# Performance work log

Measured on AMD Instinct MI355X. Metric: run time of the kernel, lower is better.

The kernel has to match this reference:

```python
import jax, jax.numpy as jnp
import numpy as np

H = 12
DH = 64
R = 8
LN_EPS = 1e-12


def setup_inputs() -> dict:
    key = jax.random.key(0)
    ks = jax.random.split(key, 6)
    B, T, D = 32, 512, 768
    s = 0.02  # realistic init scale so softmax/LN stay well-conditioned
    return {
        "hidden_states": jax.random.normal(ks[0], (B, T, D), jnp.float32),
        "Wq": jax.random.normal(ks[1], (D, D), jnp.float32) * s,
        "bq": jnp.zeros((D,), jnp.float32),
        "Wk": jax.random.normal(ks[2], (D, D), jnp.float32) * s,
        "bk": jnp.zeros((D,), jnp.float32),
        "Wv": jax.random.normal(ks[3], (D, D), jnp.float32) * s,
        "bv": jnp.zeros((D,), jnp.float32),
        "Wo": jax.random.normal(ks[4], (D, D), jnp.float32) * s,
        "bo": jnp.zeros((D,), jnp.float32),
        "ln_g": jnp.ones((D,), jnp.float32),
        "ln_b": jnp.zeros((D,), jnp.float32),
    }


def _bipartite_indices(metric, r):
    # metric: (B, T, dh); cosine-sim bipartite matching between even (a) and odd (b) tokens
    m = metric / (jnp.linalg.norm(metric, axis=-1, keepdims=True) + 1e-6)
    a, b = m[:, ::2], m[:, 1::2]
    scores = jnp.einsum('bad,bcd->bac', a, b)  # (B, Ta, Tb)
    node_max = scores.max(axis=-1)
    node_idx = scores.argmax(axis=-1)
    node_max = node_max.at[:, 0].set(-jnp.inf)  # protect CLS (a[0])
    r = min(r, a.shape[1] - 1)
    sorted_idx = jnp.argsort(-node_max, axis=-1)  # descending
    src_idx = sorted_idx[:, :r]
    unm_idx = sorted_idx[:, r:]
    dst_idx = jnp.take_along_axis(node_idx, src_idx, axis=-1)
    return src_idx, unm_idx, dst_idx


def _merge(x, src_idx, unm_idx, dst_idx):
    # x: (B, T, C) -> (B, T - r, C); scatter-mean matched even tokens into odd tokens
    src, dst = x[:, ::2], x[:, 1::2]
    matched = jnp.take_along_axis(src, src_idx[:, :, None], axis=1)  # (B, r, C)

    def scat(d, di, mm):
        sums = jnp.zeros_like(d).at[di].add(mm)
        cnt = jnp.zeros((d.shape[0],), d.dtype).at[di].add(jnp.ones(di.shape, d.dtype))
        # torch scatter_reduce 'mean' with include_self=True: (self + sum) / (1 + count)
        return (d + sums) / (1.0 + cnt[:, None])

    dst = jax.vmap(scat)(dst, dst_idx, matched)
    unm = jnp.take_along_axis(src, unm_idx[:, :, None], axis=1)
    return jnp.concatenate([unm, dst], axis=1)


def reference(hidden_states, Wq, bq, Wk, bk, Wv, bv, Wo, bo, ln_g, ln_b):
    B, T, D = hidden_states.shape

    def split_heads(x):
        return x.reshape(B, T, H, DH).transpose(0, 2, 1, 3)  # (B, H, T, dh)

    residual = hidden_states
    q = split_heads(hidden_states @ Wq + bq)
    k = split_heads(hidden_states @ Wk + bk)
    v = split_heads(hidden_states @ Wv + bv)

    # ToMe: match on head-averaged keys (computed under no_grad in torch)
    metric = jax.lax.stop_gradient(k.mean(axis=1))  # (B, T, dh)
    src_idx, unm_idx, dst_idx = _bipartite_indices(metric, R)

    def merge_heads(x):
        Bx, Hx, Tx, dx = x.shape
        y = x.transpose(0, 2, 1, 3).reshape(Bx, Tx, Hx * dx)
        y = _merge(y, src_idx, unm_idx, dst_idx)
        return y.reshape(Bx, y.shape[1], Hx, dx).transpose(0, 2, 1, 3)

    q = merge_heads(q)
    k = merge_heads(k)
    v = merge_heads(v)
    residual = _merge(residual, src_idx, unm_idx, dst_idx)

    scores = jnp.einsum('bhqd,bhkd->bhqk', q, k) / jnp.sqrt(jnp.float32(DH))
    probs = jax.nn.softmax(scores, axis=-1)  # dropout is identity in eval
    ctx = jnp.einsum('bhqk,bhkd->bhqd', probs, v)
    T2 = ctx.shape[2]
    ctx = ctx.transpose(0, 2, 1, 3).reshape(B, T2, D)
    out = ctx @ Wo + bo

    x = out + residual
    mu = x.mean(axis=-1, keepdims=True)
    var = x.var(axis=-1, keepdims=True)
    return (x - mu) / jnp.sqrt(var + LN_EPS) * ln_g + ln_b
```

## Files before the change

### kernel.cpp

```cpp
#include <hip/hip_runtime.h>
#include <math.h>

#define BNUM 32
#define TT   512
#define DD   768
#define HH   12
#define DHH  64
#define RR   8
#define TSRC 256
#define UNM  248
#define TM   504
#define MROW 16128

typedef unsigned short u16;
typedef unsigned int   u32;
typedef __attribute__((ext_vector_type(8))) short bfrag;
typedef __attribute__((ext_vector_type(4))) float ffrag;

__device__ __forceinline__ u16 f2bf(float f) {
  u32 u = __float_as_uint(f);
  u = (u + 0x7fffu + ((u >> 16) & 1u)) >> 16;
  return (u16)u;
}
__device__ __forceinline__ u32 pack2bf(float a, float b) {
  u32 ua = __float_as_uint(a), ub = __float_as_uint(b);
  ua += 0x7fffu + ((ua >> 16) & 1u);
  ub += 0x7fffu + ((ub >> 16) & 1u);
  return (ua >> 16) | (ub & 0xffff0000u);
}
__device__ __forceinline__ float bf2f(u16 v) {
  return __uint_as_float(((u32)v) << 16);
}

__device__ __forceinline__ void gl2lds16(const u16* g, u16* l) {
  __builtin_amdgcn_global_load_lds(
      (const __attribute__((address_space(1))) void*)(g),
      (__attribute__((address_space(3))) void*)(l), 16, 0, 0);
}

__global__ __launch_bounds__(256) void wkr_kernel(
    const float* __restrict__ Wk, const float* __restrict__ bk,
    float* __restrict__ Wkr, float* __restrict__ bkr) {
  int idx = blockIdx.x * 256 + threadIdx.x;
  int d = idx >> 6, j = idx & 63;
  float s = 0.f;
  #pragma unroll
  for (int h = 0; h < HH; ++h) s += Wk[(size_t)d * DD + h * DHH + j];
  Wkr[idx] = s * (1.f / 12.f);
  if (idx < 64) {
    float sb = 0.f;
    #pragma unroll
    for (int h = 0; h < HH; ++h) sb += bk[h * DHH + idx];
    bkr[idx] = sb * (1.f / 12.f);
  }
}

__global__ __launch_bounds__(256) void gemm_f32_kernel(
    const float* __restrict__ A, const float* __restrict__ W,
    const float* __restrict__ bias, float* __restrict__ C,
    int M, int N, int K) {
  __shared__ float As[32][68];
  __shared__ float Ws[32][68];
  const int t  = threadIdx.x;
  const int m0 = blockIdx.x * 64;
  const int tx = t & 15, ty = t >> 4;
  const int a_kk = t & 31;
  const int a_m  = t >> 5;
  const int w_n  = t & 63;
  const int w_k0 = t >> 6;

  float a_pre[8], w_pre[8];
  #pragma unroll
  for (int l = 0; l < 8; ++l)
    a_pre[l] = A[(size_t)(m0 + a_m + 8 * l) * K + a_kk];
  #pragma unroll
  for (int l = 0; l < 8; ++l)
    w_pre[l] = W[(size_t)(w_k0 * 8 + l) * N + w_n];

  float acc[4][4];
  #pragma unroll
  for (int i = 0; i < 4; ++i)
    #pragma unroll
    for (int j = 0; j < 4; ++j) acc[i][j] = 0.f;

  for (int k0 = 0; k0 < K; k0 += 32) {
    __syncthreads();
    #pragma unroll
    for (int l = 0; l < 8; ++l) As[a_kk][a_m + 8 * l] = a_pre[l];
    #pragma unroll
    for (int l = 0; l < 8; ++l) Ws[w_k0 * 8 + l][w_n] = w_pre[l];
    __syncthreads();
    if (k0 + 32 < K) {
      #pragma unroll
      for (int l = 0; l < 8; ++l)
        a_pre[l] = A[(size_t)(m0 + a_m + 8 * l) * K + k0 + 32 + a_kk];
      #pragma unroll
      for (int l = 0; l < 8; ++l)
        w_pre[l] = W[(size_t)(k0 + 32 + w_k0 * 8 + l) * N + w_n];
    }
    #pragma unroll
    for (int kk = 0; kk < 32; ++kk) {
      float4 a4 = *(const float4*)&As[kk][ty * 4];
      float4 w4 = *(const float4*)&Ws[kk][tx * 4];
      acc[0][0] += a4.x * w4.x; acc[0][1] += a4.x * w4.y;
      acc[0][2] += a4.x * w4.z; acc[0][3] += a4.x * w4.w;
      acc[1][0] += a4.y * w4.x; acc[1][1] += a4.y * w4.y;
      acc[1][2] += a4.y * w4.z; acc[1][3] += a4.y * w4.w;
      acc[2][0] += a4.z * w4.x; acc[2][1] += a4.z * w4.y;
      acc[2][2] += a4.z * w4.z; acc[2][3] += a4.z * w4.w;
      acc[3][0] += a4.w * w4.x; acc[3][1] += a4.w * w4.y;
      acc[3][2] += a4.w * w4.z; acc[3][3] += a4.w * w4.w;
    }
  }
  const float4 b4 = *(const float4*)&bias[tx * 4];
  #pragma unroll
  for (int i = 0; i < 4; ++i) {
    float4 v;
    v.x = acc[i][0] + b4.x; v.y = acc[i][1] + b4.y;
    v.z = acc[i][2] + b4.z; v.w = acc[i][3] + b4.w;
    *(float4*)&C[(size_t)(m0 + ty * 4 + i) * N + tx * 4] = v;
  }
}

__global__ __launch_bounds__(256) void wconv_kernel(
    const float* __restrict__ W0, const float* __restrict__ W1,
    const float* __restrict__ W2, const float* __restrict__ W3,
    u16* __restrict__ T0, u16* __restrict__ T1,
    u16* __restrict__ T2, u16* __restrict__ T3) {
  __shared__ float tile[64][65];
  int wi = blockIdx.z;
  const float* W = (wi == 0) ? W0 : (wi == 1) ? W1 : (wi == 2) ? W2 : W3;
  u16* T = (wi == 0) ? T0 : (wi == 1) ? T1 : (wi == 2) ? T2 : T3;
  int k0 = blockIdx.x * 64, n0 = blockIdx.y * 64;
  int t = threadIdx.x;
  int r = t >> 2, c4 = (t & 3) * 16;
  #pragma unroll
  for (int j = 0; j < 16; j += 4) {
    float4 v = *(const float4*)&W[(size_t)(k0 + r) * DD + n0 + c4 + j];
    tile[r][c4 + j] = v.x; tile[r][c4 + j + 1] = v.y;
    tile[r][c4 + j + 2] = v.z; tile[r][c4 + j + 3] = v.w;
  }
  __syncthreads();
  #pragma unroll
  for (int j = 0; j < 16; j += 2) {
    u32 p = (u32)f2bf(tile[c4 + j][r]) | ((u32)f2bf(tile[c4 + j + 1][r]) << 16);
    *(u32*)&T[(size_t)(n0 + r) * DD + k0 + c4 + j] = p;
  }
}

template <bool OUT_BF16, bool ADD_RES, bool ROW_BIAS, bool QK>
__global__ __launch_bounds__(256, 4) void mfma_gemm_kernel(
    const u16* __restrict__ A, const u16* __restrict__ BT,
    const float* __restrict__ bias, const float* __restrict__ bias2,
    const float* __restrict__ Res,
    float* __restrict__ Cf, u16* __restrict__ Cb, u16* __restrict__ Cb2,
    int M, int N, int K) {
  __shared__ u16 Als[2][128 * 32];
  __shared__ u16 Bls[2][128 * 32];
  const int t  = threadIdx.x;

  const int nwg = gridDim.x * gridDim.y;
  int id = blockIdx.x + blockIdx.y * gridDim.x;
  {
    const int qq = nwg >> 3, rr = nwg & 7;
    const int xcd = id & 7, pos = id >> 3;
    id = (xcd < rr) ? (xcd * (qq + 1) + pos)
                    : (rr * (qq + 1) + (xcd - rr) * qq + pos);
  }
  const int m0 = (id % gridDim.x) * 128;
  const int n0 = (id / gridDim.x) * 128;

  const int lane = t & 63;
  const int w  = t >> 6;
  const int wm = w & 1, wn = w >> 1;
  const int q  = lane >> 4;
  const int lr = lane & 15;

  const int srow = lane >> 2;
  const int schk = (lane & 3) ^ ((lane >> 3) & 3);
  const u16* gA = A  + (size_t)(m0 + w * 32 + srow) * K + schk * 8;
  const u16* gB = BT + (size_t)(n0 + w * 32 + srow) * K + schk * 8;

  const int ceff = q ^ ((lr >> 1) & 3);

  const float* biasp = bias;
  u16* Cbp = Cb;
  int n0c = n0;
  if (QK && n0 >= DD) { biasp = bias2; Cbp = Cb2; n0c = n0 - DD; }

  ffrag acc[4][4];
  #pragma unroll
  for (int i = 0; i < 4; ++i)
    #pragma unroll
    for (int j = 0; j < 4; ++j) {
      acc[i][j].x = 0.f; acc[i][j].y = 0.f; acc[i][j].z = 0.f; acc[i][j].w = 0.f;
    }

  auto STAGE = [&](int buf, int k0) {
    #pragma unroll
    for (int i = 0; i < 2; ++i) {
      gl2lds16(gA + (size_t)(i * 16) * K + k0, &Als[buf][(w * 32 + i * 16) * 32]);
      gl2lds16(gB + (size_t)(i * 16) * K + k0, &Bls[buf][(w * 32 + i * 16) * 32]);
    }
  };

  STAGE(0, 0);
  __syncthreads();

  const int NK = K >> 5;
  for (int kt = 0; kt < NK; ++kt) {
    const int cur = kt & 1;
    if (kt + 1 < NK) STAGE(cur ^ 1, (kt + 1) << 5);

    bfrag af[4], bfv[4];
    #pragma unroll
    for (int mi = 0; mi < 4; ++mi)
      af[mi] = *(const bfrag*)&Als[cur][((wm * 4 + mi) * 64 + lr * 4 + ceff) * 8];
    #pragma unroll
    for (int ni = 0; ni < 4; ++ni)
      bfv[ni] = *(const bfrag*)&Bls[cur][((wn * 4 + ni) * 64 + lr * 4 + ceff) * 8];
    #pragma unroll
    for (int mi = 0; mi < 4; ++mi)
      #pragma unroll
      for (int ni = 0; ni < 4; ++ni)
        acc[mi][ni] = __builtin_amdgcn_mfma_f32_16x16x32_bf16(
            af[mi], bfv[ni], acc[mi][ni], 0, 0, 0);

    __syncthreads();
  }

  float bcol[4];
  if (!ROW_BIAS) {
    #pragma unroll
    for (int ni = 0; ni < 4; ++ni)
      bcol[ni] = biasp[n0c + wn * 64 + ni * 16 + lr];
  }

  #pragma unroll
  for (int mi = 0; mi < 4; ++mi) {
    #pragma unroll
    for (int ni = 0; ni < 4; ++ni) {
      int gcol = n0c + wn * 64 + ni * 16 + lr;
      #pragma unroll
      for (int r = 0; r < 4; ++r) {
        int grow = m0 + wm * 64 + mi * 16 + q * 4 + r;
        size_t off = (size_t)grow * N + gcol;
        float v = acc[mi][ni][r];
        v += ROW_BIAS ? bias[grow] : bcol[ni];
        if (ADD_RES) v += Res[off];
        if (OUT_BF16) Cbp[off] = f2bf(v);
        else          Cf[off] = v;
      }
    }
  }
}

__global__ __launch_bounds__(256) void tome_scores_kernel(
    const float* __restrict__ metric, float* __restrict__ node_max,
    int* __restrict__ node_idx) {
  __shared__ float Bs[128][68];
  const int blk = blockIdx.x;
  const int b = blk >> 3, g = blk & 7;
  const int t = threadIdx.x;
  const int r = t >> 3, cc = t & 7;
  const int arow = g * 32 + r;
  const float* Mb = metric + (size_t)b * TT * 64;

  float areg[64];
  float na = 0.f;
  #pragma unroll
  for (int d4 = 0; d4 < 16; ++d4) {
    float4 v = *(const float4*)&Mb[(size_t)(2 * arow) * 64 + d4 * 4];
    areg[4 * d4 + 0] = v.x; areg[4 * d4 + 1] = v.y;
    areg[4 * d4 + 2] = v.z; areg[4 * d4 + 3] = v.w;
    na += v.x * v.x; na += v.y * v.y; na += v.z * v.z; na += v.w * v.w;
  }
  float ia = 1.f / (sqrtf(na) + 1e-6f);
  #pragma unroll
  for (int d = 0; d < 64; ++d) areg[d] *= ia;

  float best = -INFINITY; int besti = 0;
  for (int p = 0; p < 2; ++p) {
    __syncthreads();
    if (t < 128) {
      int c = p * 128 + t;
      const float* src = &Mb[(size_t)(2 * c + 1) * 64];
      float nb = 0.f;
      #pragma unroll
      for (int d4 = 0; d4 < 16; ++d4) {
        float4 v = *(const float4*)&src[d4 * 4];
        *(float4*)&Bs[t][d4 * 4] = v;
        nb += v.x * v.x; nb += v.y * v.y; nb += v.z * v.z; nb += v.w * v.w;
      }
      float ib = 1.f / (sqrtf(nb) + 1e-6f);
      #pragma unroll
      for (int d4 = 0; d4 < 16; ++d4) {
        float4 v = *(float4*)&Bs[t][d4 * 4];
        v.x *= ib; v.y *= ib; v.z *= ib; v.w *= ib;
        *(float4*)&Bs[t][d4 * 4] = v;
      }
    }
    __syncthreads();
    for (int j = 0; j < 16; ++j) {
      int cl = cc + 8 * j;
      float s = 0.f;
      #pragma unroll
      for (int d4 = 0; d4 < 16; ++d4) {
        float4 bv = *(const float4*)&Bs[cl][d4 * 4];
        s += areg[4 * d4 + 0] * bv.x; s += areg[4 * d4 + 1] * bv.y;
        s += areg[4 * d4 + 2] * bv.z; s += areg[4 * d4 + 3] * bv.w;
      }
      int c = p * 128 + cl;
      if (s > best) { best = s; besti = c; }
    }
  }
  #pragma unroll
  for (int off = 1; off < 8; off <<= 1) {
    float bm = __shfl_xor(best, off);
    int   bi = __shfl_xor(besti, off);
    if (bm > best || (bm == best && bi < besti)) { best = bm; besti = bi; }
  }
  if (cc == 0) {
    node_max[b * TSRC + arow] = best;
    node_idx[b * TSRC + arow] = besti;
  }
}

__global__ __launch_bounds__(256) void tome_rank_kernel(
    const float* __restrict__ node_max, const int* __restrict__ node_idx,
    int* __restrict__ order_g, int* __restrict__ dst_g) {
  __shared__ float km[TSRC];
  __shared__ int ord[TSRC];
  int b = blockIdx.x, i = threadIdx.x;
  float best = (i == 0) ? -INFINITY : node_max[b * TSRC + i];
  km[i] = best;
  __syncthreads();
  float ki = km[i];
  int r = 0;
  for (int j = 0; j < TSRC; ++j) {
    float kj = km[j];
    if (kj > ki || (kj == ki && j < i)) ++r;
  }
  ord[r] = i;
  __syncthreads();
  order_g[b * TSRC + i] = ord[i];
  if (i < RR) dst_g[b * RR + i] = node_idx[b * TSRC + ord[i]];
}

__global__ __launch_bounds__(256) void merge_kernel(
    const float* __restrict__ X, const int* __restrict__ order,
    const int* __restrict__ dsti, float* __restrict__ Xm,
    u16* __restrict__ Xmb) {
  int row = blockIdx.x;
  int b = row / TM, t2 = row % TM;
  int c = threadIdx.x;
  const float* Xb = X + (size_t)b * TT * DD;
  float out[3];
  if (t2 < UNM) {
    int tok = 2 * order[b * TSRC + RR + t2];
    #pragma unroll
    for (int l = 0; l < 3; ++l) out[l] = Xb[(size_t)tok * DD + c + 256 * l];
  } else {
    int j = t2 - UNM;
    float cnt = 1.f;
    #pragma unroll
    for (int l = 0; l < 3; ++l) out[l] = Xb[(size_t)(2 * j + 1) * DD + c + 256 * l];
    for (int m = 0; m < RR; ++m) {
      if (dsti[b * RR + m] == j) {
        int tok = 2 * order[b * TSRC + m];
        #pragma unroll
        for (int l = 0; l < 3; ++l) out[l] += Xb[(size_t)tok * DD + c + 256 * l];
        cnt += 1.f;
      }
    }
    float inv = 1.f / cnt;
    #pragma unroll
    for (int l = 0; l < 3; ++l) out[l] *= inv;
  }
  #pragma unroll
  for (int l = 0; l < 3; ++l) {
    Xm[(size_t)row * DD + c + 256 * l]  = out[l];
    Xmb[(size_t)row * DD + c + 256 * l] = f2bf(out[l]);
  }
}

#define NQT 8
__global__ __launch_bounds__(256) void attn_kernel(
    const u16* __restrict__ Q, const u16* __restrict__ K,
    const u16* __restrict__ VT, u16* __restrict__ ctx) {
  __shared__ u16 Kls[2][64][64];
  __shared__ u16 Vls[2][64][64];
  __shared__ u16 Pt[64][72];

  int blk = blockIdx.x;
  int bh = blk % (BNUM * HH);
  int qt = blk / (BNUM * HH);
  int h = bh % HH, b = bh / HH;
  const int t = threadIdx.x;
  const int lane = t & 63, w = t >> 6;
  const int lr = lane & 15, quad = lane >> 4;
  const int q0 = qt * 64;
  const size_t base = (size_t)b * TM * DD + (size_t)h * DHH;

  bfrag qf[2];
  {
    const u16* qp = Q + base + (size_t)(q0 + 16 * w + lr) * DD + quad * 8;
    qf[0] = *(const bfrag*)(qp);
    qf[1] = *(const bfrag*)(qp + 32);
  }

  const int srow = lane >> 3;
  const int schk = (lane & 7) ^ srow;
  const u16* Kg = K + base + (size_t)schk * 8;
  const u16* Vg0 = VT + (size_t)(h * DHH + w * 16 + srow) * MROW + (size_t)b * TM;
  const u16* Vg1 = Vg0 + (size_t)8 * MROW;

  const int cA = (quad)     ^ (lr & 7);
  const int cB = (quad + 4) ^ (lr & 7);

  float m_i = -INFINITY, l_i = 0.f;
  ffrag o[4];
  #pragma unroll
  for (int ni = 0; ni < 4; ++ni) {
    o[ni].x = 0.f; o[ni].y = 0.f; o[ni].z = 0.f; o[ni].w = 0.f;
  }

  auto STAGE = [&](int cur, int kt) {
    const int k0s = kt * 64;
    int t0 = k0s + w * 16 + srow;
    int t1 = t0 + 8;
    t0 = (t0 < TM) ? t0 : (TM - 1);
    t1 = (t1 < TM) ? t1 : (TM - 1);
    gl2lds16(Kg + (size_t)t0 * DD, &Kls[cur][w * 16][0]);
    gl2lds16(Kg + (size_t)t1 * DD, &Kls[cur][w * 16 + 8][0]);
    int tb = k0s + schk * 8;
    tb = (tb <= TM - 8) ? tb : (TM - 8);
    gl2lds16(Vg0 + tb, &Vls[cur][w * 16][0]);
    gl2lds16(Vg1 + tb, &Vls[cur][w * 16 + 8][0]);
  };

  STAGE(0, 0);
  __syncthreads();

  const float L2E = 1.4426950408889634f;
  const float C1  = 0.125f * 1.4426950408889634f;

  #pragma unroll
  for (int kt = 0; kt < NQT; ++kt) {
    const int cur = kt & 1;

    if (kt + 1 < NQT) STAGE(cur ^ 1, kt + 1);

    ffrag s4[4];
    __builtin_amdgcn_s_setprio(1);
    #pragma unroll
    for (int mi = 0; mi < 4; ++mi) {
      bfrag ka0 = *(const bfrag*)&Kls[cur][mi * 16 + lr][cA * 8];
      bfrag ka1 = *(const bfrag*)&Kls[cur][mi * 16 + lr][cB * 8];
      ffrag z; z.x = 0.f; z.y = 0.f; z.z = 0.f; z.w = 0.f;
      z = __builtin_amdgcn_mfma_f32_16x16x32_bf16(ka0, qf[0], z, 0, 0, 0);
      s4[mi] = __builtin_amdgcn_mfma_f32_16x16x32_bf16(ka1, qf[1], z, 0, 0, 0);
    }
    __builtin_amdgcn_s_setprio(0);

    if (kt == NQT - 1) {
      #pragma unroll
      for (int mi = 0; mi < 4; ++mi)
        #pragma unroll
        for (int r = 0; r < 4; ++r) {
          int rel = mi * 16 + quad * 4 + r;
          if (mi == 3)
            s4[mi][r] = (448 + rel < TM) ? s4[mi][r] : -INFINITY;
        }
    }

    float mx01 = fmaxf(fmaxf(s4[0][0], s4[0][1]), fmaxf(s4[0][2], s4[0][3]));
    float mx23 = fmaxf(fmaxf(s4[1][0], s4[1][1]), fmaxf(s4[1][2], s4[1][3]));
    float mx45 = fmaxf(fmaxf(s4[2][0], s4[2][1]), fmaxf(s4[2][2], s4[2][3]));
    float mx67 = fmaxf(fmaxf(s4[3][0], s4[3][1]), fmaxf(s4[3][2], s4[3][3]));
    float rmax = fmaxf(fmaxf(mx01, mx23), fmaxf(mx45, mx67));
    rmax = fmaxf(rmax, __shfl_xor(rmax, 16));
    rmax = fmaxf(rmax, __shfl_xor(rmax, 32));
    float pmax = rmax * 0.125f;

    if (!__all(pmax <= m_i + 8.f)) {
      float nm = fmaxf(m_i, pmax);
      float alpha = __builtin_amdgcn_exp2f((m_i - nm) * L2E);
      float al[4];
      #pragma unroll
      for (int r = 0; r < 4; ++r) al[r] = __shfl(alpha, quad * 4 + r);
      #pragma unroll
      for (int ni = 0; ni < 4; ++ni)
        #pragma unroll
        for (int r = 0; r < 4; ++r) o[ni][r] *= al[r];
      l_i *= alpha;
      m_i = nm;
    }
    float nml2 = m_i * L2E;

    float p[16];
    float pa0 = 0.f, pa1 = 0.f, pa2 = 0.f, pa3 = 0.f;
    #pragma unroll
    for (int mi = 0; mi < 4; ++mi)
      #pragma unroll
      for (int r = 0; r < 4; ++r) {
        float e = __builtin_amdgcn_exp2f(__builtin_fmaf(s4[mi][r], C1, -nml2));
        p[mi * 4 + r] = e;
        if (r == 0) pa0 += e; else if (r == 1) pa1 += e;
        else if (r == 2) pa2 += e; else pa3 += e;
      }
    float psum = (pa0 + pa1) + (pa2 + pa3);
    psum += __shfl_xor(psum, 16);
    psum += __shfl_xor(psum, 32);
    l_i += psum;

    #pragma unroll
    for (int mi = 0; mi < 4; ++mi) {
      u32 lo = pack2bf(p[mi * 4 + 0], p[mi * 4 + 1]);
      u32 hi = pack2bf(p[mi * 4 + 2], p[mi * 4 + 3]);
      u32* dst = (u32*)&Pt[16 * w + lr][mi * 16 + quad * 4];
      dst[0] = lo; dst[1] = hi;
    }

    bfrag pfa0 = *(const bfrag*)&Pt[16 * w + lr][quad * 8];
    bfrag pfa1 = *(const bfrag*)&Pt[16 * w + lr][32 + quad * 8];
    __builtin_amdgcn_s_setprio(1);
    #pragma unroll
    for (int ni = 0; ni < 4; ++ni) {
      bfrag vb0 = *(const bfrag*)&Vls[cur][ni * 16 + lr][cA * 8];
      bfrag vb1 = *(const bfrag*)&Vls[cur][ni * 16 + lr][cB * 8];
      o[ni] = __builtin_amdgcn_mfma_f32_16x16x32_bf16(pfa0, vb0, o[ni], 0, 0, 0);
      o[ni] = __builtin_amdgcn_mfma_f32_16x16x32_bf16(pfa1, vb1, o[ni], 0, 0, 0);
    }
    __builtin_amdgcn_s_setprio(0);

    __syncthreads();
  }

  float invl[4];
  #pragma unroll
  for (int r = 0; r < 4; ++r) {
    float lv = __shfl(l_i, quad * 4 + r);
    invl[r] = 1.f / lv;
  }
  #pragma unroll
  for (int r = 0; r < 4; ++r) {
    int row = q0 + 16 * w + quad * 4 + r;
    if (row < TM) {
      size_t g = base + (size_t)row * DD + lr;
      #pragma unroll
      for (int ni = 0; ni < 4; ++ni)
        ctx[g + ni * 16] = f2bf(o[ni][r] * invl[r]);
    }
  }
}

__global__ __launch_bounds__(256) void ln_kernel(
    float* __restrict__ Y, const float* __restrict__ g,
    const float* __restrict__ beta) {
  __shared__ float red[4];
  int row = blockIdx.x, t = threadIdx.x;
  size_t baseo = (size_t)row * DD;
  float x[3];
  #pragma unroll
  for (int l = 0; l < 3; ++l) x[l] = Y[baseo + t + 256 * l];
  float s = x[0] + x[1] + x[2];
  #pragma unroll
  for (int off = 32; off > 0; off >>= 1) s += __shfl_down(s, off, 64);
  if ((t & 63) == 0) red[t >> 6] = s;
  __syncthreads();
  float mu = (red[0] + red[1] + red[2] + red[3]) * (1.f / 768.f);
  __syncthreads();
  float d0 = x[0] - mu, d1 = x[1] - mu, d2 = x[2] - mu;
  float sq = d0 * d0 + d1 * d1 + d2 * d2;
  #pragma unroll
  for (int off = 32; off > 0; off >>= 1) sq += __shfl_down(sq, off, 64);
  if ((t & 63) == 0) red[t >> 6] = sq;
  __syncthreads();
  float var = (red[0] + red[1] + red[2] + red[3]) * (1.f / 768.f);
  float inv = rsqrtf(var + 1e-12f);
  #pragma unroll
  for (int l = 0; l < 3; ++l) {
    int c = t + 256 * l;
    Y[baseo + c] = (x[l] - mu) * inv * g[c] + beta[c];
  }
}

extern "C" void kernel_launch(void* const* d_in, const int* in_sizes, int n_in,
                              void* d_out, int out_size, void* d_ws, size_t ws_size,
                              hipStream_t stream) {
  const float* X    = (const float*)d_in[0];
  const float* Wq   = (const float*)d_in[1];
  const float* bq   = (const float*)d_in[2];
  const float* Wk   = (const float*)d_in[3];
  const float* bk   = (const float*)d_in[4];
  const float* Wv   = (const float*)d_in[5];
  const float* bv   = (const float*)d_in[6];
  const float* Wo   = (const float*)d_in[7];
  const float* bo   = (const float*)d_in[8];
  const float* ln_g = (const float*)d_in[9];
  const float* ln_b = (const float*)d_in[10];
  float* out = (float*)d_out;

  const size_t metric_n = (size_t)16384 * 64;
  const size_t wkr_n    = (size_t)768 * 64 + 64;
  const size_t idx_n    = (size_t)BNUM * TSRC + BNUM * RR;
  const size_t nm_n     = (size_t)2 * BNUM * TSRC;
  const size_t buf_n    = (size_t)MROW * DD;
  const size_t w_n      = (size_t)DD * DD;
  const size_t f32_elems = metric_n + wkr_n + idx_n + nm_n + buf_n;
  const size_t u16_elems = 4 * buf_n + 4 * w_n;
  const size_t needed = f32_elems * 4 + u16_elems * 2;
  if (ws_size < needed) return;

  float* ws = (float*)d_ws;
  float* metric   = ws;
  float* Wkr      = metric + metric_n;
  float* bkr      = Wkr + (size_t)768 * 64;
  int*   order_g  = (int*)(bkr + 64);
  int*   dst_g    = order_g + BNUM * TSRC;
  float* node_max = (float*)(dst_g + BNUM * RR);
  int*   node_idx = (int*)(node_max + BNUM * TSRC);
  float* Xm       = (float*)(node_idx + BNUM * TSRC);
  u16*   Xmb      = (u16*)(Xm + buf_n);
  u16*   Qmb      = Xmb + buf_n;
  u16*   Kmb      = Qmb + buf_n;
  u16*   VTb      = Kmb + buf_n;
  u16*   WqT      = VTb + buf_n;
  u16*   WkT      = WqT + w_n;
  u16*   WvT      = WkT + w_n;
  u16*   WoT      = WvT + w_n;
  u16*   ctxb     = Qmb;

  wkr_kernel<<<(768 * 64) / 256, 256, 0, stream>>>(Wk, bk, Wkr, bkr);
  wconv_kernel<<<dim3(12, 12, 4), 256, 0, stream>>>(
      Wq, Wk, Wv, Wo, WqT, WkT, WvT, WoT);
  gemm_f32_kernel<<<dim3(16384 / 64, 1), 256, 0, stream>>>(
      X, Wkr, bkr, metric, 16384, 64, 768);
  tome_scores_kernel<<<BNUM * 8, 256, 0, stream>>>(metric, node_max, node_idx);
  tome_rank_kernel<<<BNUM, 256, 0, stream>>>(node_max, node_idx, order_g, dst_g);
  merge_kernel<<<MROW, 256, 0, stream>>>(X, order_g, dst_g, Xm, Xmb);
  mfma_gemm_kernel<true, false, false, true>
      <<<dim3(MROW / 128, 2 * DD / 128), 256, 0, stream>>>(
      Xmb, WqT, bq, bk, nullptr, nullptr, Qmb, Kmb, MROW, DD, DD);
  mfma_gemm_kernel<true, false, true, false>
      <<<dim3(DD / 128, MROW / 128), 256, 0, stream>>>(
      WvT, Xmb, bv, nullptr, nullptr, nullptr, VTb, nullptr, DD, MROW, DD);
  attn_kernel<<<BNUM * HH * NQT, 256, 0, stream>>>(Qmb, Kmb, VTb, ctxb);
  mfma_gemm_kernel<false, true, false, false>
      <<<dim3(MROW / 128, DD / 128), 256, 0, stream>>>(
      ctxb, WoT, bo, nullptr, Xm, out, nullptr, nullptr, MROW, DD, DD);
  ln_kernel<<<MROW, 256, 0, stream>>>(out, ln_g, ln_b);
}
```

Before: 398.7 us.

## Feed softmax probabilities to PV MFMA from registers, dropping LDS round-trip

Removes the Pt shared-memory staging buffer in the attention kernel. The packed bf16 probabilities stay in registers and are used directly as the MFMA A operand. To make that work, V is now read from LDS with a permuted k-index layout, two 8-byte reads per fragment, so its layout matches the register layout of P. It also raises the occupancy hint to 5 blocks per SM on both the GEMM and attention kernels, which may force register spills.

Measured after the change: 417.0 us. +4.6%, slower.

```diff
diff --git a/kernel.cpp b/kernel.cpp
--- a/kernel.cpp
+++ b/kernel.cpp
@@ -16,6 +16,7 @@
 typedef unsigned int   u32;
 typedef __attribute__((ext_vector_type(8))) short bfrag;
 typedef __attribute__((ext_vector_type(4))) float ffrag;
+typedef __attribute__((ext_vector_type(2))) unsigned int u32x2;
 
 __device__ __forceinline__ u16 f2bf(float f) {
   u32 u = __float_as_uint(f);
@@ -149,7 +150,7 @@
 }
 
 template <bool OUT_BF16, bool ADD_RES, bool ROW_BIAS, bool QK>
-__global__ __launch_bounds__(256, 4) void mfma_gemm_kernel(
+__global__ __launch_bounds__(256, 5) void mfma_gemm_kernel(
     const u16* __restrict__ A, const u16* __restrict__ BT,
     const float* __restrict__ bias, const float* __restrict__ bias2,
     const float* __restrict__ Res,
@@ -385,12 +386,11 @@
 }
 
 #define NQT 8
-__global__ __launch_bounds__(256) void attn_kernel(
+__global__ __launch_bounds__(256, 5) void attn_kernel(
     const u16* __restrict__ Q, const u16* __restrict__ K,
     const u16* __restrict__ VT, u16* __restrict__ ctx) {
   __shared__ u16 Kls[2][64][64];
   __shared__ u16 Vls[2][64][64];
-  __shared__ u16 Pt[64][72];
 
   int blk = blockIdx.x;
   int bh = blk % (BNUM * HH);
@@ -417,6 +417,7 @@
 
   const int cA = (quad)     ^ (lr & 7);
   const int cB = (quad + 4) ^ (lr & 7);
+  const int vq = quad >> 1, vh = (quad & 1) * 4, lx = lr & 7;
 
   float m_i = -INFINITY, l_i = 0.f;
   ffrag o[4];
@@ -514,23 +515,30 @@
     psum += __shfl_xor(psum, 32);
     l_i += psum;
 
+    u32 pk[8];
     #pragma unroll
     for (int mi = 0; mi < 4; ++mi) {
-      u32 lo = pack2bf(p[mi * 4 + 0], p[mi * 4 + 1]);
-      u32 hi = pack2bf(p[mi * 4 + 2], p[mi * 4 + 3]);
-      u32* dst = (u32*)&Pt[16 * w + lr][mi * 16 + quad * 4];
-      dst[0] = lo; dst[1] = hi;
-    }
-
-    bfrag pfa0 = *(const bfrag*)&Pt[16 * w + lr][quad * 8];
-    bfrag pfa1 = *(const bfrag*)&Pt[16 * w + lr][32 + quad * 8];
+      pk[2 * mi]     = pack2bf(p[mi * 4 + 0], p[mi * 4 + 1]);
+      pk[2 * mi + 1] = pack2bf(p[mi * 4 + 2], p[mi * 4 + 3]);
+    }
+
     __builtin_amdgcn_s_setprio(1);
     #pragma unroll
-    for (int ni = 0; ni < 4; ++ni) {
-      bfrag vb0 = *(const bfrag*)&Vls[cur][ni * 16 + lr][cA * 8];
-      bfrag vb1 = *(const bfrag*)&Vls[cur][ni * 16 + lr][cB * 8];
-      o[ni] = __builtin_amdgcn_mfma_f32_16x16x32_bf16(pfa0, vb0, o[ni], 0, 0, 0);
-      o[ni] = __builtin_amdgcn_mfma_f32_16x16x32_bf16(pfa1, vb1, o[ni], 0, 0, 0);
+    for (int mh = 0; mh < 2; ++mh) {
+      union { u32 u[4]; bfrag f; } pa;
+      pa.u[0] = pk[4 * mh + 0]; pa.u[1] = pk[4 * mh + 1];
+      pa.u[2] = pk[4 * mh + 2]; pa.u[3] = pk[4 * mh + 3];
+      const int c0 = ((4 * mh + vq) ^ lx) * 8 + vh;
+      const int c1 = ((4 * mh + 2 + vq) ^ lx) * 8 + vh;
+      #pragma unroll
+      for (int ni = 0; ni < 4; ++ni) {
+        const u16* vp = &Vls[cur][ni * 16 + lr][0];
+        u32x2 v0 = *(const u32x2*)(vp + c0);
+        u32x2 v1 = *(const u32x2*)(vp + c1);
+        union { u32 u[4]; bfrag f; } vb;
+        vb.u[0] = v0.x; vb.u[1] = v0.y; vb.u[2] = v1.x; vb.u[3] = v1.y;
+        o[ni] = __builtin_amdgcn_mfma_f32_16x16x32_bf16(pa.f, vb.f, o[ni], 0, 0, 0);
+      }
     }
     __builtin_amdgcn_s_setprio(0);
 
```
